# Kernel optimization log

Hardware: AMD Instinct MI355X
Metric: run time of the kernel (lower is better)

Reference implementation:

```python
import jax, jax.numpy as jnp
import numpy as np

DIM = 1024
AUX = 3
B, S = 32, 1024
ENC_D = DIM * AUX  # 3072


def setup_inputs() -> dict:
    key = jax.random.key(0)
    ks = jax.random.split(key, 5)
    sc1 = 1.0 / np.sqrt(DIM * (AUX + 1))
    sc3 = 1.0 / np.sqrt(ENC_D)
    return {
        "hidden_state": jax.random.normal(ks[0], (B, DIM), jnp.float32),
        "encoder_outputs": jax.random.normal(ks[1], (B, S, ENC_D), jnp.float32),
        "W1": jax.random.normal(ks[2], (DIM, DIM * (AUX + 1)), jnp.float32) * sc1,
        "b1": jnp.zeros((DIM,), jnp.float32),
        "w2": jax.random.normal(ks[3], (1, DIM), jnp.float32) * (1.0 / np.sqrt(DIM)),
        "W3": jax.random.normal(ks[4], (DIM, ENC_D), jnp.float32) * sc3,
        "b3": jnp.zeros((DIM,), jnp.float32),
    }


def reference(hidden_state, encoder_outputs, W1, b1, w2, W3, b3):
    # hidden_state: (B, dim); encoder_outputs: (B, S, dim*aux)
    Bsz, Slen, _ = encoder_outputs.shape
    h = jnp.broadcast_to(hidden_state[:, None, :], (Bsz, Slen, hidden_state.shape[-1]))
    inputs = jnp.concatenate([encoder_outputs, h], axis=2)  # (B, S, dim*(aux+1))
    # score MLP: tanh(linear1) -> linear2 (no bias)
    hidden = jnp.tanh(jnp.einsum('bsf,df->bsd', inputs, W1) + b1)  # (B, S, dim)
    e = jnp.einsum('bsd,od->bso', hidden, w2)[..., 0]  # (B, S)
    alpha = jax.nn.softmax(e, axis=1)
    context = jnp.einsum('bs,bsf->bf', alpha, encoder_outputs)  # (B, dim*aux)
    return jnp.einsum('bf,df->bd', context, W3) + b3  # (B, dim)
```

## Files before the change

### kernel.cpp

```cpp
#include <hip/hip_runtime.h>
#include <hip/hip_bf16.h>


typedef float          fx4 __attribute__((ext_vector_type(4)));
typedef short          sv8 __attribute__((ext_vector_type(8)));
typedef unsigned short uv4 __attribute__((ext_vector_type(4)));
typedef unsigned int   ui4 __attribute__((ext_vector_type(4)));

__device__ __forceinline__ unsigned short f2bf(float x) {
  unsigned u = __float_as_uint(x);
  return (unsigned short)((u + 0x7FFFu + ((u >> 16) & 1u)) >> 16);
}

__device__ __forceinline__ unsigned cvtpk(float lo, float hi) {
  unsigned r;
  asm("v_cvt_pk_bf16_f32 %0, %1, %2" : "=v"(r) : "v"(lo), "v"(hi));
  return r;
}
__device__ __forceinline__ ui4 pack8(fx4 a, fx4 b) {
  ui4 v;
  v[0] = cvtpk(a[0], a[1]); v[1] = cvtpk(a[2], a[3]);
  v[2] = cvtpk(b[0], b[1]); v[3] = cvtpk(b[2], b[3]);
  return v;
}

__global__ void convw1_kernel(const float* __restrict__ W1, unsigned short* __restrict__ W1a) {
  int id = blockIdx.x * 256 + threadIdx.x;
  int d = id / 768, fi = id - d * 768;
  fx4 v = ((const fx4*)W1)[d * 1024 + fi];
  uv4 r; r[0] = f2bf(v[0]); r[1] = f2bf(v[1]); r[2] = f2bf(v[2]); r[3] = f2bf(v[3]);
  ((uv4*)W1a)[d * 768 + fi] = r;
}

__global__ void hbias_kernel(const float* __restrict__ hs, const float* __restrict__ W1,
                             const float* __restrict__ b1, float* __restrict__ hb) {
  int idx = (blockIdx.x << 2) + (threadIdx.x >> 6);
  int lane = threadIdx.x & 63;
  int b = idx >> 10, d = idx & 1023;
  const fx4* hv = (const fx4*)hs;
  const fx4* wv = (const fx4*)W1;
  float s = 0.f;
#pragma unroll
  for (int i = 0; i < 4; ++i) {
    int k4 = lane + (i << 6);
    fx4 h = hv[(b << 8) + k4];
    fx4 w = wv[d * 1024 + 768 + k4];
    s += h[0] * w[0] + h[1] * w[1] + h[2] * w[2] + h[3] * w[3];
  }
#pragma unroll
  for (int off = 32; off; off >>= 1) s += __shfl_xor(s, off);
  if (lane == 0) hb[idx] = s + b1[d];
}

__global__ __launch_bounds__(256, 3)
void gemm_score(const float* __restrict__ enc,
                const unsigned short* __restrict__ W1a,
                const float* __restrict__ hb,
                const float* __restrict__ w2,
                float* __restrict__ pe) {
  __shared__ __align__(16) unsigned short As[2][4096];
  __shared__ __align__(16) unsigned short Bs[2][4096];

  const int t = threadIdx.x;
  const int lane = t & 63, wid = t >> 6;
  const int wm = wid >> 1, wn = wid & 1;

  const int bid = blockIdx.x;
  const int lg = ((bid & 7) << 8) | (bid >> 3);
  const int mt = lg >> 3, ntile = lg & 7;
  const int row0 = mt << 7;
  const int col0 = ntile << 7;

  const fx4* encv = (const fx4*)enc;

  const int ar = t >> 1, ah = t & 1;
  const int agb = (row0 + ar) * 768 + ah * 4;
  const int awb = ar * 32;
  const int ws0 = (((ah << 1) + 0) ^ (ar & 3)) << 3;
  const int ws1 = (((ah << 1) + 1) ^ (ar & 3)) << 3;

  const int bcl = (wid << 4) + (lane >> 2);
  const int bsw = (((lane & 3) ^ ((lane >> 2) & 3)) << 3);
  const unsigned short* bsrc0 = W1a + (col0 + bcl) * 3072 + bsw;
  const unsigned short* bsrc1 = W1a + (col0 + 64 + bcl) * 3072 + bsw;
  const int bdst0 = bcl << 5;
  const int bdst1 = (64 + bcl) << 5;

  const int r15 = lane & 15, qv = lane >> 4;
  const int offA = (wm * 64 + r15) * 32 + ((qv ^ (r15 & 3)) << 3);
  const int offB = (wn * 64 + r15) * 32 + ((qv ^ (r15 & 3)) << 3);

  fx4 acc[4][4] = {};
  fx4 pa[4];

#define A_LOAD(kt) { _Pragma("unroll") for (int j = 0; j < 4; ++j) pa[j] = encv[agb + (kt) * 8 + j]; }
#define A_WRITE(bq) { *(ui4*)&As[bq][awb + ws0] = pack8(pa[0], pa[1]); \
                      *(ui4*)&As[bq][awb + ws1] = pack8(pa[2], pa[3]); }
#define B_ISSUE(bq, kt)                                               \
  { __builtin_amdgcn_global_load_lds(                                 \
        (const __attribute__((address_space(1))) void*)(bsrc0 + (kt) * 32), \
        (__attribute__((address_space(3))) void*)&Bs[bq][bdst0], 16, 0, 0); \
    __builtin_amdgcn_global_load_lds(                                 \
        (const __attribute__((address_space(1))) void*)(bsrc1 + (kt) * 32), \
        (__attribute__((address_space(3))) void*)&Bs[bq][bdst1], 16, 0, 0); }
#define COMPUTE(p)                                                    \
  { sv8 af[4], bfv[4];                                                \
    _Pragma("unroll")                                                 \
    for (int mi = 0; mi < 4; ++mi) af[mi] = *(const sv8*)&As[p][offA + mi * 512]; \
    _Pragma("unroll")                                                 \
    for (int ni = 0; ni < 4; ++ni) bfv[ni] = *(const sv8*)&Bs[p][offB + ni * 512]; \
    _Pragma("unroll")                                                 \
    for (int mi = 0; mi < 4; ++mi)                                    \
      _Pragma("unroll")                                               \
      for (int ni = 0; ni < 4; ++ni)                                  \
        acc[mi][ni] = __builtin_amdgcn_mfma_f32_16x16x32_bf16(af[mi], bfv[ni], acc[mi][ni], 0, 0, 0); }
#define ITER(kt, p)                                                   \
  { COMPUTE(p)                                                        \
    if ((kt) < 95) { A_WRITE(p ^ 1) }       \
    if ((kt) < 94) { A_LOAD((kt) + 2) }                               \
    __builtin_amdgcn_s_barrier();            \
    if ((kt) < 94) {                                                  \
      B_ISSUE(p, (kt) + 2)                                            \
      asm volatile("s_waitcnt vmcnt(6)" ::: "memory");                \
    } else if ((kt) == 94) {                                          \
      asm volatile("s_waitcnt vmcnt(0)" ::: "memory");                \
    }                                                                 \
    asm volatile("s_waitcnt lgkmcnt(0)" ::: "memory");                \
    __builtin_amdgcn_s_barrier(); }

  A_LOAD(0)
  B_ISSUE(0, 0)
  A_WRITE(0)
  A_LOAD(1)
  B_ISSUE(1, 1)
  asm volatile("s_waitcnt vmcnt(6)" ::: "memory");
  asm volatile("s_waitcnt lgkmcnt(0)" ::: "memory");
  __builtin_amdgcn_s_barrier();

  for (int kt2 = 0; kt2 < 48; ++kt2) {
    const int kt = kt2 * 2;
    ITER(kt, 0)
    ITER(kt + 1, 1)
  }

  const int b = row0 >> 10;
  float w2v[4], hbv[4];
#pragma unroll
  for (int ni = 0; ni < 4; ++ni) {
    int c = col0 + wn * 64 + ni * 16 + r15;
    w2v[ni] = w2[c];
    hbv[ni] = hb[(b << 10) + c];
  }
#pragma unroll
  for (int mi = 0; mi < 4; ++mi) {
#pragma unroll
    for (int j = 0; j < 4; ++j) {
      float pz = 0.f;
#pragma unroll
      for (int ni = 0; ni < 4; ++ni)
        pz += tanhf(acc[mi][ni][j] + hbv[ni]) * w2v[ni];
      pz += __shfl_xor(pz, 1); pz += __shfl_xor(pz, 2);
      pz += __shfl_xor(pz, 4); pz += __shfl_xor(pz, 8);
      if (r15 == 0) {
        int row = row0 + wm * 64 + mi * 16 + (qv << 2) + j;
        pe[(row << 4) + (ntile << 1) + wn] = pz;
      }
    }
  }
#undef A_LOAD
#undef A_WRITE
#undef B_ISSUE
#undef COMPUTE
#undef ITER
}

__global__ void softmax_kernel(const float* __restrict__ pe, float* __restrict__ alpha) {
  int b = blockIdx.x, t = threadIdx.x;
  int lane = t & 63, wid = t >> 6;
  float ev[4];
#pragma unroll
  for (int r = 0; r < 4; ++r) {
    int s = t + r * 256;
    const float* p = pe + ((b << 10) + s) * 16;
    float sum = 0.f;
#pragma unroll
    for (int i = 0; i < 16; ++i) sum += p[i];
    ev[r] = sum;
  }
  float m = fmaxf(fmaxf(ev[0], ev[1]), fmaxf(ev[2], ev[3]));
#pragma unroll
  for (int off = 32; off; off >>= 1) m = fmaxf(m, __shfl_xor(m, off));
  __shared__ float red[8];
  if (lane == 0) red[wid] = m;
  __syncthreads();
  m = fmaxf(fmaxf(red[0], red[1]), fmaxf(red[2], red[3]));
  float p4[4], ls = 0.f;
#pragma unroll
  for (int r = 0; r < 4; ++r) { p4[r] = expf(ev[r] - m); ls += p4[r]; }
#pragma unroll
  for (int off = 32; off; off >>= 1) ls += __shfl_xor(ls, off);
  if (lane == 0) red[4 + wid] = ls;
  __syncthreads();
  float inv = 1.0f / (red[4] + red[5] + red[6] + red[7]);
#pragma unroll
  for (int r = 0; r < 4; ++r) alpha[(b << 10) + t + r * 256] = p4[r] * inv;
}

__global__ void ctxpart_kernel(const float* __restrict__ enc, const float* __restrict__ alpha,
                               float* __restrict__ part) {
  int bid = blockIdx.x, b = bid >> 4, sc = bid & 15;
  int t = threadIdx.x;
  __shared__ float sal[64];
  if (t < 64) sal[t] = alpha[(b << 10) + (sc << 6) + t];
  __syncthreads();
  const fx4* ev = (const fx4*)enc;
  fx4 a0 = {}, a1 = {}, a2 = {};
  int base = ((b << 10) + (sc << 6)) * 768;
  for (int si = 0; si < 64; ++si) {
    float a = sal[si];
    const fx4* rp = ev + base + si * 768;
    a0 += a * rp[t];
    a1 += a * rp[256 + t];
    a2 += a * rp[512 + t];
  }
  fx4* pp = (fx4*)part;
  int pb = ((b << 4) + sc) * 768;
  pp[pb + t] = a0; pp[pb + 256 + t] = a1; pp[pb + 512 + t] = a2;
}

__global__ void ctxreduce_kernel(const float* __restrict__ part, float* __restrict__ ctx) {
  int j = blockIdx.x * 256 + threadIdx.x;
  int b = j / 768, fi = j - b * 768;
  const fx4* pp = (const fx4*)part;
  fx4 s = {};
#pragma unroll
  for (int i = 0; i < 16; ++i) s += pp[((b << 4) + i) * 768 + fi];
  ((fx4*)ctx)[b * 768 + fi] = s;
}

__global__ void final_kernel(const float* __restrict__ ctx, const float* __restrict__ W3,
                             const float* __restrict__ b3, float* __restrict__ out) {
  int idx = (blockIdx.x << 2) + (threadIdx.x >> 6);
  int lane = threadIdx.x & 63;
  int b = idx >> 10, d = idx & 1023;
  const fx4* cv = (const fx4*)ctx;
  const fx4* wv = (const fx4*)W3;
  float s = 0.f;
#pragma unroll
  for (int i = 0; i < 12; ++i) {
    int f4 = lane + (i << 6);
    fx4 c = cv[b * 768 + f4];
    fx4 w = wv[d * 768 + f4];
    s += c[0] * w[0] + c[1] * w[1] + c[2] * w[2] + c[3] * w[3];
  }
#pragma unroll
  for (int off = 32; off; off >>= 1) s += __shfl_xor(s, off);
  if (lane == 0) out[idx] = s + b3[d];
}

extern "C" void kernel_launch(void* const* d_in, const int* in_sizes, int n_in,
                              void* d_out, int out_size, void* d_ws, size_t ws_size,
                              hipStream_t stream) {
  const float* hs  = (const float*)d_in[0];
  const float* enc = (const float*)d_in[1];
  const float* W1  = (const float*)d_in[2];
  const float* b1  = (const float*)d_in[3];
  const float* w2  = (const float*)d_in[4];
  const float* W3  = (const float*)d_in[5];
  const float* b3  = (const float*)d_in[6];
  float* out = (float*)d_out;

  char* ws = (char*)d_ws;
  unsigned short* W1a = (unsigned short*)(ws);
  float* pe    = (float*)(ws + 6291456);
  float* alpha = (float*)(ws + 8388608);
  float* hb    = (float*)(ws + 8519680);
  float* ctx   = (float*)(ws + 8650752);
  float* part  = (float*)(ws + 9043968);

  convw1_kernel<<<3072, 256, 0, stream>>>(W1, W1a);
  hbias_kernel<<<8192, 256, 0, stream>>>(hs, W1, b1, hb);
  gemm_score<<<2048, 256, 0, stream>>>(enc, W1a, hb, w2, pe);
  softmax_kernel<<<32, 256, 0, stream>>>(pe, alpha);
  ctxpart_kernel<<<512, 256, 0, stream>>>(enc, alpha, part);
  ctxreduce_kernel<<<96, 256, 0, stream>>>(part, ctx);
  final_kernel<<<8192, 256, 0, stream>>>(ctx, W3, b3, out);
}
```

Measured before the change: 500.4 us.

## Stream fp32 encoder tiles into LDS via direct loads with 256x128 tiles

The score GEMM now uses 512-thread blocks computing 256x128 tiles with a 64-wide K step. Both the fp32 encoder operand and the bf16 weights are loaded straight into LDS with global_load_lds, and the bf16 conversion of A moves to after the LDS read. This removes the register-staged A path (global load, convert, LDS write) and gains operand reuse from the larger tile. It also adds s_setprio around the MFMA blocks. In exchange, LDS use roughly triples because A is stored as fp32, the grid is half as large, and each thread does more conversion work per MFMA.

```diff
diff --git a/kernel.cpp b/kernel.cpp
--- a/kernel.cpp
+++ b/kernel.cpp
@@ -17,11 +17,11 @@
   asm("v_cvt_pk_bf16_f32 %0, %1, %2" : "=v"(r) : "v"(lo), "v"(hi));
   return r;
 }
-__device__ __forceinline__ ui4 pack8(fx4 a, fx4 b) {
+__device__ __forceinline__ sv8 pack8s(fx4 a, fx4 b) {
   ui4 v;
   v[0] = cvtpk(a[0], a[1]); v[1] = cvtpk(a[2], a[3]);
   v[2] = cvtpk(b[0], b[1]); v[3] = cvtpk(b[2], b[3]);
-  return v;
+  sv8 r; __builtin_memcpy(&r, &v, 16); return r;
 }
 
 __global__ void convw1_kernel(const float* __restrict__ W1, unsigned short* __restrict__ W1a) {
@@ -52,95 +52,106 @@
   if (lane == 0) hb[idx] = s + b1[d];
 }
 
-__global__ __launch_bounds__(256, 3)
+__global__ __launch_bounds__(512, 2)
 void gemm_score(const float* __restrict__ enc,
                 const unsigned short* __restrict__ W1a,
                 const float* __restrict__ hb,
                 const float* __restrict__ w2,
                 float* __restrict__ pe) {
-  __shared__ __align__(16) unsigned short As[2][4096];
-  __shared__ __align__(16) unsigned short Bs[2][4096];
+  __shared__ __align__(16) float As[2][2][8192];
+  __shared__ __align__(16) unsigned short Bs[2][8192];
 
   const int t = threadIdx.x;
   const int lane = t & 63, wid = t >> 6;
   const int wm = wid >> 1, wn = wid & 1;
 
   const int bid = blockIdx.x;
-  const int lg = ((bid & 7) << 8) | (bid >> 3);
+  const int lg = ((bid & 7) << 7) | (bid >> 3);
   const int mt = lg >> 3, ntile = lg & 7;
-  const int row0 = mt << 7;
+  const int row0 = mt << 8;
   const int col0 = ntile << 7;
 
-  const fx4* encv = (const fx4*)enc;
-
-  const int ar = t >> 1, ah = t & 1;
-  const int agb = (row0 + ar) * 768 + ah * 4;
-  const int awb = ar * 32;
-  const int ws0 = (((ah << 1) + 0) ^ (ar & 3)) << 3;
-  const int ws1 = (((ah << 1) + 1) ^ (ar & 3)) << 3;
-
-  const int bcl = (wid << 4) + (lane >> 2);
-  const int bsw = (((lane & 3) ^ ((lane >> 2) & 3)) << 3);
-  const unsigned short* bsrc0 = W1a + (col0 + bcl) * 3072 + bsw;
-  const unsigned short* bsrc1 = W1a + (col0 + 64 + bcl) * 3072 + bsw;
-  const int bdst0 = bcl << 5;
-  const int bdst1 = (64 + bcl) << 5;
-
-  const int r15 = lane & 15, qv = lane >> 4;
-  const int offA = (wm * 64 + r15) * 32 + ((qv ^ (r15 & 3)) << 3);
-  const int offB = (wn * 64 + r15) * 32 + ((qv ^ (r15 & 3)) << 3);
+  const int l3 = lane >> 3, l7 = lane & 7;
+  const float* aptr = enc + (size_t)(row0 + wid * 32 + l3) * 3072 + ((l7 ^ l3) << 2);
+  const unsigned short* bptr = W1a + (size_t)(col0 + wid * 16 + l3) * 3072 + ((l7 ^ l3) << 3);
+
+  const int r15 = lane & 15, qv = lane >> 4, r7s = r15 & 7;
+  const int aro = (wm * 64 + r15) * 32;
+  const int sA0 = ((2 * qv) ^ r7s) << 2;
+  const int sA1 = ((2 * qv + 1) ^ r7s) << 2;
+  const int bco = (wn * 64 + r15) * 64;
+  const int sB0 = (qv ^ r7s) << 3;
+  const int sB1 = ((qv + 4) ^ r7s) << 3;
 
   fx4 acc[4][4] = {};
-  fx4 pa[4];
-
-#define A_LOAD(kt) { _Pragma("unroll") for (int j = 0; j < 4; ++j) pa[j] = encv[agb + (kt) * 8 + j]; }
-#define A_WRITE(bq) { *(ui4*)&As[bq][awb + ws0] = pack8(pa[0], pa[1]); \
-                      *(ui4*)&As[bq][awb + ws1] = pack8(pa[2], pa[3]); }
-#define B_ISSUE(bq, kt)                                               \
-  { __builtin_amdgcn_global_load_lds(                                 \
-        (const __attribute__((address_space(1))) void*)(bsrc0 + (kt) * 32), \
-        (__attribute__((address_space(3))) void*)&Bs[bq][bdst0], 16, 0, 0); \
-    __builtin_amdgcn_global_load_lds(                                 \
-        (const __attribute__((address_space(1))) void*)(bsrc1 + (kt) * 32), \
-        (__attribute__((address_space(3))) void*)&Bs[bq][bdst1], 16, 0, 0); }
-#define COMPUTE(p)                                                    \
-  { sv8 af[4], bfv[4];                                                \
-    _Pragma("unroll")                                                 \
-    for (int mi = 0; mi < 4; ++mi) af[mi] = *(const sv8*)&As[p][offA + mi * 512]; \
-    _Pragma("unroll")                                                 \
-    for (int ni = 0; ni < 4; ++ni) bfv[ni] = *(const sv8*)&Bs[p][offB + ni * 512]; \
-    _Pragma("unroll")                                                 \
+
+#define A_ISSUE(buf, kh, kt)                                          \
+  { _Pragma("unroll")                                                 \
+    for (int i = 0; i < 4; ++i)                                       \
+      __builtin_amdgcn_global_load_lds(                               \
+        (const __attribute__((address_space(1))) void*)(aptr + i * 24576 + (kt) * 64 + (kh) * 32), \
+        (__attribute__((address_space(3))) void*)&As[buf][kh][(wid * 32 + i * 8) * 32], 16, 0, 0); }
+#define B_ISSUE(buf, kt)                                              \
+  { _Pragma("unroll")                                                 \
+    for (int i = 0; i < 2; ++i)                                       \
+      __builtin_amdgcn_global_load_lds(                               \
+        (const __attribute__((address_space(1))) void*)(bptr + i * 24576 + (kt) * 64), \
+        (__attribute__((address_space(3))) void*)&Bs[buf][(wid * 16 + i * 8) * 64], 16, 0, 0); }
+#define MFMA16                                                        \
+  __builtin_amdgcn_s_setprio(1);                                      \
+  { _Pragma("unroll")                                                 \
     for (int mi = 0; mi < 4; ++mi)                                    \
       _Pragma("unroll")                                               \
       for (int ni = 0; ni < 4; ++ni)                                  \
-        acc[mi][ni] = __builtin_amdgcn_mfma_f32_16x16x32_bf16(af[mi], bfv[ni], acc[mi][ni], 0, 0, 0); }
-#define ITER(kt, p)                                                   \
-  { COMPUTE(p)                                                        \
-    if ((kt) < 95) { A_WRITE(p ^ 1) }       \
-    if ((kt) < 94) { A_LOAD((kt) + 2) }                               \
-    __builtin_amdgcn_s_barrier();            \
-    if ((kt) < 94) {                                                  \
-      B_ISSUE(p, (kt) + 2)                                            \
-      asm volatile("s_waitcnt vmcnt(6)" ::: "memory");                \
-    } else if ((kt) == 94) {                                          \
-      asm volatile("s_waitcnt vmcnt(0)" ::: "memory");                \
+        acc[mi][ni] = __builtin_amdgcn_mfma_f32_16x16x32_bf16(af[mi], bfv[ni], acc[mi][ni], 0, 0, 0); } \
+  __builtin_amdgcn_s_setprio(0);
+
+#define PH1(kt, bp)                                                   \
+  { sv8 af[4], bfv[4];                                                \
+    _Pragma("unroll")                                                 \
+    for (int mi = 0; mi < 4; ++mi) {                                  \
+      fx4 x = *(const fx4*)&As[bp][0][aro + mi * 512 + sA0];          \
+      fx4 y = *(const fx4*)&As[bp][0][aro + mi * 512 + sA1];          \
+      af[mi] = pack8s(x, y);                                          \
     }                                                                 \
+    _Pragma("unroll")                                                 \
+    for (int ni = 0; ni < 4; ++ni)                                    \
+      bfv[ni] = *(const sv8*)&Bs[bp][bco + ni * 1024 + sB0];          \
+    if ((kt) < 47) { B_ISSUE((bp) ^ 1, (kt) + 1) }                    \
+    __builtin_amdgcn_s_barrier();                                     \
     asm volatile("s_waitcnt lgkmcnt(0)" ::: "memory");                \
+    MFMA16                                                            \
     __builtin_amdgcn_s_barrier(); }
 
-  A_LOAD(0)
+#define PH2(kt, bp)                                                   \
+  { sv8 af[4], bfv[4];                                                \
+    _Pragma("unroll")                                                 \
+    for (int mi = 0; mi < 4; ++mi) {                                  \
+      fx4 x = *(const fx4*)&As[bp][1][aro + mi * 512 + sA0];          \
+      fx4 y = *(const fx4*)&As[bp][1][aro + mi * 512 + sA1];          \
+      af[mi] = pack8s(x, y);                                          \
+    }                                                                 \
+    _Pragma("unroll")                                                 \
+    for (int ni = 0; ni < 4; ++ni)                                    \
+      bfv[ni] = *(const sv8*)&Bs[bp][bco + ni * 1024 + sB1];          \
+    __builtin_amdgcn_s_barrier();         \
+    if ((kt) < 46) { A_ISSUE(bp, 0, (kt) + 2) A_ISSUE(bp, 1, (kt) + 2) } \
+    asm volatile("s_waitcnt lgkmcnt(0)" ::: "memory");                \
+    MFMA16                                                            \
+    if ((kt) < 46)       { asm volatile("s_waitcnt vmcnt(8)" ::: "memory"); } \
+    else if ((kt) == 46) { asm volatile("s_waitcnt vmcnt(0)" ::: "memory"); } \
+    __builtin_amdgcn_s_barrier(); }
+
+  A_ISSUE(0, 0, 0) A_ISSUE(0, 1, 0)
   B_ISSUE(0, 0)
-  A_WRITE(0)
-  A_LOAD(1)
-  B_ISSUE(1, 1)
-  asm volatile("s_waitcnt vmcnt(6)" ::: "memory");
-  asm volatile("s_waitcnt lgkmcnt(0)" ::: "memory");
+  A_ISSUE(1, 0, 1) A_ISSUE(1, 1, 1)
+  asm volatile("s_waitcnt vmcnt(8)" ::: "memory");
   __builtin_amdgcn_s_barrier();
 
-  for (int kt2 = 0; kt2 < 48; ++kt2) {
-    const int kt = kt2 * 2;
-    ITER(kt, 0)
-    ITER(kt + 1, 1)
+  for (int tt = 0; tt < 24; ++tt) {
+    const int kt = tt * 2;
+    PH1(kt, 0) PH2(kt, 0)
+    PH1(kt + 1, 1) PH2(kt + 1, 1)
   }
 
   const int b = row0 >> 10;
@@ -167,11 +178,11 @@
       }
     }
   }
-#undef A_LOAD
-#undef A_WRITE
+#undef A_ISSUE
 #undef B_ISSUE
-#undef COMPUTE
-#undef ITER
+#undef MFMA16
+#undef PH1
+#undef PH2
 }
 
 __global__ void softmax_kernel(const float* __restrict__ pe, float* __restrict__ alpha) {
@@ -280,7 +291,7 @@
 
   convw1_kernel<<<3072, 256, 0, stream>>>(W1, W1a);
   hbias_kernel<<<8192, 256, 0, stream>>>(hs, W1, b1, hb);
-  gemm_score<<<2048, 256, 0, stream>>>(enc, W1a, hb, w2, pe);
+  gemm_score<<<1024, 512, 0, stream>>>(enc, W1a, hb, w2, pe);
   softmax_kernel<<<32, 256, 0, stream>>>(pe, alpha);
   ctxpart_kernel<<<512, 256, 0, stream>>>(enc, alpha, part);
   ctxreduce_kernel<<<96, 256, 0, stream>>>(part, ctx);
```

Result: slower. 538.9 us (+7.7%).
